# Kernel optimization log

Hardware: AMD Instinct MI355X
Metric: run time of the kernel (lower is better)

Reference implementation:

```python
import jax, jax.numpy as jnp
import numpy as np

B, L, T_ENC = 32, 64, 196
INPUT, EMBED, HIDDEN, VOCAB = 2048, 512, 512, 32000
SCALE = 1.0 / float(512 ** 0.5)


def setup_inputs() -> dict:
    key = jax.random.key(0)
    ks = jax.random.split(key, 24)
    s = 0.05
    embed_table = jax.random.normal(ks[3], (VOCAB, EMBED)) * s
    embed_table = embed_table.at[0].set(0.0)  # padding_idx=0
    d = {
        "features": jax.random.normal(ks[0], (B, INPUT)),
        "captions": jax.random.randint(ks[1], (B, L), 0, VOCAB, dtype=jnp.int32),
        "lengths": jnp.full((B,), L, dtype=jnp.int32),
        "encoder_outputs": jax.random.normal(ks[2], (B, T_ENC, 512)),
        "embed_table": embed_table,
        "ft1_w": jax.random.normal(ks[4], (HIDDEN, INPUT)) * s,
        "ft1_b": jax.random.normal(ks[5], (HIDDEN,)) * s,
        "ft2_w": jax.random.normal(ks[6], (HIDDEN, HIDDEN)) * s,
        "ft2_b": jax.random.normal(ks[7], (HIDDEN,)) * s,
        # torch LSTM gate order: i, f, g, o; layer0 input = embed+512
        "w_ih0": jax.random.normal(ks[8], (4 * HIDDEN, EMBED + 512)) * s,
        "w_hh0": jax.random.normal(ks[9], (4 * HIDDEN, HIDDEN)) * s,
        "b_ih0": jax.random.normal(ks[10], (4 * HIDDEN,)) * s,
        "b_hh0": jax.random.normal(ks[11], (4 * HIDDEN,)) * s,
        "w_ih1": jax.random.normal(ks[12], (4 * HIDDEN, HIDDEN)) * s,
        "w_hh1": jax.random.normal(ks[13], (4 * HIDDEN, HIDDEN)) * s,
        "b_ih1": jax.random.normal(ks[14], (4 * HIDDEN,)) * s,
        "b_hh1": jax.random.normal(ks[15], (4 * HIDDEN,)) * s,
        "fc_w": jax.random.normal(ks[16], (VOCAB, HIDDEN)) * s,
        "fc_b": jax.random.normal(ks[17], (VOCAB,)) * s,
    }
    return d


def _lstm_cell(x, h, c, w_ih, w_hh, b_ih, b_hh):
    g = x @ w_ih.T + h @ w_hh.T + b_ih + b_hh
    i, f, gg, o = jnp.split(g, 4, axis=-1)
    c2 = jax.nn.sigmoid(f) * c + jax.nn.sigmoid(i) * jnp.tanh(gg)
    h2 = jax.nn.sigmoid(o) * jnp.tanh(c2)
    return h2, c2


def reference(features, captions, lengths, encoder_outputs, embed_table,
              ft1_w, ft1_b, ft2_w, ft2_b,
              w_ih0, w_hh0, b_ih0, b_hh0,
              w_ih1, w_hh1, b_ih1, b_hh1,
              fc_w, fc_b):
    # feature extractor (eval mode -> dropout identity)
    f = jax.nn.relu(features @ ft1_w.T + ft1_b)
    f = f @ ft2_w.T + ft2_b                      # [B, H]
    h0 = jnp.stack([f, f])                       # [num_layers, B, H]
    c0 = h0

    emb = embed_table[captions]                  # [B, L, E]
    xs = jnp.swapaxes(emb, 0, 1)                 # [L, B, E]

    def step(carry, w):
        h, c = carry
        q = h[-1]                                             # [B, 512]
        scores = jnp.einsum('bh,bth->bt', q, encoder_outputs) * SCALE
        a = jax.nn.softmax(scores, axis=-1)
        ctx = jnp.einsum('bt,bth->bh', a, encoder_outputs)    # [B, 512]
        x = jnp.concatenate([w, ctx], axis=-1)                # [B, E+512]
        h0n, c0n = _lstm_cell(x, h[0], c[0], w_ih0, w_hh0, b_ih0, b_hh0)
        h1n, c1n = _lstm_cell(h0n, h[1], c[1], w_ih1, w_hh1, b_ih1, b_hh1)
        return (jnp.stack([h0n, h1n]), jnp.stack([c0n, c1n])), h1n

    _, hs = jax.lax.scan(step, (h0, c0), xs)      # hs: [L, B, H]
    logits = jnp.einsum('lbh,vh->lbv', hs, fc_w) + fc_b  # [L, B, V]
    # all lengths == L, so pack_padded_sequence data == time-major flatten
    return logits.reshape(L * B, VOCAB)
```

## Files before the change

### kernel.cpp

```cpp
#include <hip/hip_runtime.h>
#include <hip/hip_bf16.h>

typedef __hip_bfloat16 bf16;
typedef short s8v __attribute__((ext_vector_type(8)));
typedef float f4v __attribute__((ext_vector_type(4)));
typedef unsigned long long u64;
typedef unsigned int u32;

#define B_   32
#define L_   64
#define TENC 196
#define INP  2048
#define H_   512
#define V_   32000
#define NBLK 128

static __device__ __forceinline__ float sigf(float x) { return 1.0f / (1.0f + expf(-x)); }
static __device__ __forceinline__ short f2bs(float x) {
    bf16 h = (bf16)x;
    return *(short*)&h;
}
static __device__ __forceinline__ float b2f(short s) {
    return __uint_as_float(((unsigned int)(unsigned short)s) << 16);
}
static __device__ __forceinline__ u32 packhl(float v) {
    bf16 hi = (bf16)v;
    float r = v - (float)hi;
    bf16 lo = (bf16)r;
    return ((u32)(*(unsigned short*)&hi) << 16) | (u32)(*(unsigned short*)&lo);
}
static __device__ __forceinline__ float ldf(const void* p, size_t i, int f32) {
    if (f32) return ((const float*)p)[i];
    return (float)((const bf16*)p)[i];
}
static __device__ __forceinline__ s8v ld8(const void* p, size_t i, int f32) {
    if (f32) {
        const float* fp = (const float*)p + i;
        float4 a = *(const float4*)fp;
        float4 b = *(const float4*)(fp + 4);
        s8v r;
        r[0] = f2bs(a.x); r[1] = f2bs(a.y); r[2] = f2bs(a.z); r[3] = f2bs(a.w);
        r[4] = f2bs(b.x); r[5] = f2bs(b.y); r[6] = f2bs(b.z); r[7] = f2bs(b.w);
        return r;
    }
    return *(const s8v*)((const bf16*)p + i);
}
static __device__ __forceinline__ s8v ld8lo(const void* p, size_t i, int f32) {
    s8v r = {};
    if (f32) {
        const float* fp = (const float*)p + i;
        float4 a = *(const float4*)fp;
        float4 b = *(const float4*)(fp + 4);
        float v[8] = {a.x, a.y, a.z, a.w, b.x, b.y, b.z, b.w};
        for (int j = 0; j < 8; ++j) {
            bf16 hi = (bf16)v[j];
            bf16 lo = (bf16)(v[j] - (float)hi);
            r[j] = *(short*)&lo;
        }
    }
    return r;
}

static __device__ __forceinline__ u64 ld64coh(const void* p) {
    return __hip_atomic_load((const u64*)p, __ATOMIC_RELAXED, __HIP_MEMORY_SCOPE_AGENT);
}
static __device__ __forceinline__ void st32coh(u32* p, u32 v) {
    __hip_atomic_store(p, v, __ATOMIC_RELAXED, __HIP_MEMORY_SCOPE_AGENT);
}
static __device__ __forceinline__ void st64coh(u32* p, u64 v) {
    __hip_atomic_store((u64*)p, v, __ATOMIC_RELAXED, __HIP_MEMORY_SCOPE_AGENT);
}

static __device__ __forceinline__ void gridbar(int* cnt, int target) {
    asm volatile("s_waitcnt vmcnt(0)" ::: "memory");
    __syncthreads();
    if (threadIdx.x == 0) {
        __hip_atomic_fetch_add(cnt, 1, __ATOMIC_RELAXED, __HIP_MEMORY_SCOPE_AGENT);
        while (__hip_atomic_load(cnt, __ATOMIC_RELAXED, __HIP_MEMORY_SCOPE_AGENT) < target)
            __builtin_amdgcn_s_sleep(1);
    }
    __syncthreads();
}

static __device__ __forceinline__ void issue32(const u32* St, int tid, u64* f) {
    int b0 = (tid >> 7), k = (tid & 127) * 4;
    #pragma unroll
    for (int q = 0; q < 16; ++q) {
        const u32* s = St + (2 * q + b0) * H_ + k;
        f[2 * q]     = ld64coh(s);
        f[2 * q + 1] = ld64coh(s + 2);
    }
}
static __device__ __forceinline__ void stage_write(const u64* f, int tid, short (*A)[520]) {
    int b0 = (tid >> 7), k = (tid & 127) * 4;
    #pragma unroll
    for (int q = 0; q < 16; ++q) {
        u32 v0 = (u32)f[2 * q],     v1 = (u32)(f[2 * q] >> 32);
        u32 v2 = (u32)f[2 * q + 1], v3 = (u32)(f[2 * q + 1] >> 32);
        int b = 2 * q + b0;
        uint2 hi, lo;
        hi.x = (v0 >> 16) | (v1 & 0xffff0000u);
        hi.y = (v2 >> 16) | (v3 & 0xffff0000u);
        lo.x = (v0 & 0xffffu) | (v1 << 16);
        lo.y = (v2 & 0xffffu) | (v3 << 16);
        *(uint2*)&A[2 * b][k]     = hi;
        *(uint2*)&A[2 * b + 1][k] = lo;
    }
}
static __device__ __forceinline__ f4v mfma_half(const short (*W)[1048], const short (*A)[520],
                                                int mrow, int nlo, int kq, int koff, f4v acc) {
    #pragma unroll
    for (int kk = 0; kk < 16; ++kk) {
        s8v a = *(const s8v*)&A[mrow][kk * 32 + kq];
        s8v b = *(const s8v*)&W[nlo][koff + kk * 32 + kq];
        acc = __builtin_amdgcn_mfma_f32_16x16x32_bf16(a, b, acc, 0, 0, 0);
    }
    return acc;
}

__global__ __launch_bounds__(256) void k_detect(const void* __restrict__ feat,
                                                int* __restrict__ flag) {
    __shared__ float red[256];
    const unsigned short* p = (const unsigned short*)feat;
    float mx = 0.f;
    for (int i = threadIdx.x; i < 65536; i += 256) {
        unsigned int u = ((unsigned int)p[i]) << 16;
        float v = __uint_as_float(u);
        mx = fmaxf(mx, fabsf(v));
    }
    red[threadIdx.x] = mx;
    __syncthreads();
    for (int s = 128; s; s >>= 1) {
        if (threadIdx.x < s) red[threadIdx.x] = fmaxf(red[threadIdx.x], red[threadIdx.x + s]);
        __syncthreads();
    }
    if (threadIdx.x == 0) flag[0] = (red[0] > 1e4f) ? 1 : 0;
}

__global__ __launch_bounds__(256) void k_prep(const int* __restrict__ dflag,
                                              const void* __restrict__ enc,
                                              const void* __restrict__ w_ih0, const void* __restrict__ w_hh0,
                                              const void* __restrict__ w_ih1, const void* __restrict__ w_hh1,
                                              const void* __restrict__ b_ih0, const void* __restrict__ b_hh0,
                                              const void* __restrict__ b_ih1, const void* __restrict__ b_hh1,
                                              bf16* __restrict__ enc16,
                                              bf16* __restrict__ Wp0, bf16* __restrict__ Wp1,
                                              float* __restrict__ bias0, float* __restrict__ bias1,
                                              int* __restrict__ bar) {
    int f32 = *dflag;
    int gid = blockIdx.x * 256 + threadIdx.x;
    if (gid == 0) bar[0] = 0;
    const int GE = (B_ * TENC * H_) / 8;
    const int GW = (2048 * 1024) / 8;
    int stride = gridDim.x * 256;
    for (int g = gid; g < GE + 2 * GW; g += stride) {
        if (g < GE) {
            *(s8v*)(enc16 + (size_t)g * 8) = ld8(enc, (size_t)g * 8, f32);
        } else if (g < GE + GW) {
            int gg = g - GE; int j = gg >> 7; int k = (gg & 127) * 8;
            s8v v = (k < 512) ? ld8(w_ih0, (size_t)j * 1024 + 512 + k, f32)
                              : ld8(w_hh0, (size_t)j * 512 + (k - 512), f32);
            *(s8v*)(Wp0 + (size_t)j * 1024 + k) = v;
        } else {
            int gg = g - GE - GW; int j = gg >> 7; int k = (gg & 127) * 8;
            s8v v = (k < 512) ? ld8(w_ih1, (size_t)j * 512 + k, f32)
                              : ld8(w_hh1, (size_t)j * 512 + (k - 512), f32);
            *(s8v*)(Wp1 + (size_t)j * 1024 + k) = v;
        }
    }
    for (int j = gid; j < 2048; j += stride) {
        bias0[j] = ldf(b_ih0, j, f32) + ldf(b_hh0, j, f32);
        bias1[j] = ldf(b_ih1, j, f32) + ldf(b_hh1, j, f32);
    }
}

__global__ __launch_bounds__(256) void k_gemb(const int* __restrict__ dflag,
                                              const int* __restrict__ captions,
                                              const void* __restrict__ embed,
                                              const void* __restrict__ w_ih0,
                                              float* __restrict__ Gemb) {
    __shared__ short As[128][40];
    __shared__ short Bs[128][40];
    int f32 = *dflag;
    int n0 = blockIdx.x * 128;
    int m0 = blockIdx.y * 128;
    int tid = threadIdx.x, lane = tid & 63, wv = tid >> 6;
    int wm = wv >> 1, wn = wv & 1;
    f4v acc[16] = {};
    for (int k0 = 0; k0 < 512; k0 += 32) {
        for (int s = tid; s < 512; s += 256) {
            int r = s >> 2, cs = (s & 3) * 8;
            int R = m0 + r, e = R >> 1, part = R & 1;
            int b = e & 31, tt = e >> 5;
            size_t ei = (size_t)captions[b * L_ + tt] * H_ + k0 + cs;
            *(s8v*)&As[r][cs] = part ? ld8lo(embed, ei, f32) : ld8(embed, ei, f32);
        }
        for (int s = tid; s < 512; s += 256) {
            int r = s >> 2, cs = (s & 3) * 8;
            *(s8v*)&Bs[r][cs] = ld8(w_ih0, (size_t)(n0 + r) * 1024 + k0 + cs, f32);
        }
        __syncthreads();
        int kq = (lane >> 4) * 8;
        s8v af[4], bfv[4];
        for (int i = 0; i < 4; ++i) af[i]  = *(const s8v*)&As[wm * 64 + i * 16 + (lane & 15)][kq];
        for (int i = 0; i < 4; ++i) bfv[i] = *(const s8v*)&Bs[wn * 64 + i * 16 + (lane & 15)][kq];
        for (int mi = 0; mi < 4; ++mi)
            for (int ni = 0; ni < 4; ++ni)
                acc[mi * 4 + ni] = __builtin_amdgcn_mfma_f32_16x16x32_bf16(af[mi], bfv[ni], acc[mi * 4 + ni], 0, 0, 0);
        __syncthreads();
    }
    int n = lane & 15, quad = lane >> 4;
    for (int ni = 0; ni < 4; ++ni) {
        int col = n0 + wn * 64 + ni * 16 + n;
        for (int mi = 0; mi < 4; ++mi) {
            f4v a = acc[mi * 4 + ni];
            int rowbase = m0 + wm * 64 + mi * 16 + quad * 4;
            int e0 = rowbase >> 1;
            Gemb[(size_t)e0 * 2048 + col]       = a[0] + a[1];
            Gemb[(size_t)(e0 + 1) * 2048 + col] = a[2] + a[3];
        }
    }
}

__global__ __launch_bounds__(256) void k_feat1(const int* __restrict__ dflag,
                                               const void* __restrict__ feat,
                                               const void* __restrict__ w,
                                               const void* __restrict__ bias,
                                               float* __restrict__ t1) {
    int f32 = *dflag;
    int wid = (blockIdx.x * 256 + threadIdx.x) >> 6;
    int lane = threadIdx.x & 63;
    int b = wid >> 9, o = wid & 511;
    float acc = 0.f;
    for (int k = lane; k < INP; k += 64)
        acc += ldf(feat, (size_t)b * INP + k, f32) * ldf(w, (size_t)o * INP + k, f32);
    for (int off = 32; off; off >>= 1) acc += __shfl_down(acc, off, 64);
    if (lane == 0) {
        acc += ldf(bias, o, f32);
        t1[b * H_ + o] = acc > 0.f ? acc : 0.f;
    }
}

__global__ __launch_bounds__(256) void k_feat2(const int* __restrict__ dflag,
                                               const float* __restrict__ t1,
                                               const void* __restrict__ w,
                                               const void* __restrict__ bias,
                                               float* __restrict__ c0, float* __restrict__ c1,
                                               u32* __restrict__ h0A, u32* __restrict__ h1A) {
    int f32 = *dflag;
    int wid = (blockIdx.x * 256 + threadIdx.x) >> 6;
    int lane = threadIdx.x & 63;
    int b = wid >> 9, o = wid & 511;
    float acc = 0.f;
    for (int k = lane; k < H_; k += 64)
        acc += t1[b * H_ + k] * ldf(w, (size_t)o * H_ + k, f32);
    for (int off = 32; off; off >>= 1) acc += __shfl_down(acc, off, 64);
    if (lane == 0) {
        float v = acc + ldf(bias, o, f32);
        int idx = b * H_ + o;
        c0[idx] = v; c1[idx] = v;
        u32 pk = packhl(v);
        h0A[idx] = pk; h1A[idx] = pk;
    }
}

__global__ __launch_bounds__(256, 1) void k_recur(
        const bf16* __restrict__ enc16,
        const bf16* __restrict__ Wp0, const bf16* __restrict__ Wp1,
        const float* __restrict__ bias0, const float* __restrict__ bias1,
        const float* __restrict__ Gemb,
        const float* __restrict__ c0i, const float* __restrict__ c1i,
        u32* __restrict__ h0A, u32* __restrict__ h0B,
        u32* __restrict__ h1A, u32* __restrict__ h1B,
        u32* __restrict__ ctxp,
        bf16* __restrict__ hs, int* __restrict__ bar) {
    __shared__ short Asm[64][520];
    __shared__ short Wsm[2][16][1048];
    __shared__ float qs[H_];
    __shared__ float sc[256];
    __shared__ float wred[8];
    __shared__ float ep[4][4][32];
    const float SCALE = 0.04419417382415922f;
    int blk = blockIdx.x, tid = threadIdx.x;
    int lane = tid & 63, wv = tid >> 6;
    int u0 = blk * 4;
    int mrow = wv * 16 + (lane & 15);
    int kq = (lane >> 4) * 8;
    int nlo = lane & 15;
    int quad = lane >> 4;
    int b0i = wv * 8 + quad * 2;
    int eb = tid & 31, eu = (tid >> 5) & 3, ej = u0 + eu;
    int epi = tid < 128;

    for (int cell = 0; cell < 2; ++cell) {
        const bf16* Wp = cell ? Wp1 : Wp0;
        for (int s = tid; s < 2048; s += 256) {
            int r = s >> 7, cc = (s & 127) * 8;
            size_t j = (size_t)((r >> 2) * H_ + u0 + (r & 3));
            *(s8v*)&Wsm[cell][r][cc] = *(const s8v*)(Wp + j * 1024 + cc);
        }
    }
    float c0r = 0.f, c1r = 0.f;
    float bi0 = 0, bf0 = 0, bg0 = 0, bo0 = 0, bi1 = 0, bf1 = 0, bg1 = 0, bo1 = 0;
    if (epi) {
        c0r = c0i[eb * H_ + ej]; c1r = c1i[eb * H_ + ej];
        bi0 = bias0[ej]; bf0 = bias0[512 + ej]; bg0 = bias0[1024 + ej]; bo0 = bias0[1536 + ej];
        bi1 = bias1[ej]; bf1 = bias1[512 + ej]; bg1 = bias1[1024 + ej]; bo1 = bias1[1536 + ej];
    }
    __syncthreads();
    int nbar = 0;

    for (int t = 0; t < L_; ++t) {
        int p = t & 1;
        const u32* h0p = p ? h0B : h0A;  u32* h0n = p ? h0A : h0B;
        const u32* h1p = p ? h1B : h1A;  u32* h1n = p ? h1A : h1B;

        u64 fA[32];
        issue32(h0p, tid, fA);
        f4v accB = {};
        if (blk < B_) {
            int b = blk;
            {
                u64 v = ld64coh(h1p + b * H_ + 2 * tid);
                u32 v0 = (u32)v, v1 = (u32)(v >> 32);
                qs[2 * tid]     = b2f((short)(v0 >> 16)) + b2f((short)(v0 & 0xffffu));
                qs[2 * tid + 1] = b2f((short)(v1 >> 16)) + b2f((short)(v1 & 0xffffu));
            }
            __syncthreads();
            if (tid < TENC) {
                const bf16* erow = enc16 + ((size_t)b * TENC + tid) * H_;
                float a0 = 0, a1 = 0, a2 = 0, a3 = 0, a4 = 0, a5 = 0, a6 = 0, a7 = 0;
                #pragma unroll 4
                for (int k = 0; k < H_; k += 8) {
                    s8v e8 = *(const s8v*)(erow + k);
                    float4 q0 = *(const float4*)&qs[k];
                    float4 q1 = *(const float4*)&qs[k + 4];
                    a0 += q0.x * b2f(e8[0]); a1 += q0.y * b2f(e8[1]);
                    a2 += q0.z * b2f(e8[2]); a3 += q0.w * b2f(e8[3]);
                    a4 += q1.x * b2f(e8[4]); a5 += q1.y * b2f(e8[5]);
                    a6 += q1.z * b2f(e8[6]); a7 += q1.w * b2f(e8[7]);
                }
                sc[tid] = (((a0 + a1) + (a2 + a3)) + ((a4 + a5) + (a6 + a7))) * SCALE;
            }
            __syncthreads();
            float v = (tid < TENC) ? sc[tid] : -1e30f;
            float m = v;
            #pragma unroll
            for (int off = 32; off; off >>= 1) m = fmaxf(m, __shfl_xor(m, off, 64));
            if (lane == 0) wred[wv] = m;
            __syncthreads();
            m = fmaxf(fmaxf(wred[0], wred[1]), fmaxf(wred[2], wred[3]));
            float e = (tid < TENC) ? expf(v - m) : 0.f;
            float s = e;
            #pragma unroll
            for (int off = 32; off; off >>= 1) s += __shfl_xor(s, off, 64);
            if (lane == 0) wred[4 + wv] = s;
            __syncthreads();
            float inv = 1.0f / ((wred[4] + wred[5]) + (wred[6] + wred[7]));
            if (tid < TENC) sc[tid] = e * inv;
            __syncthreads();
            const bf16* ebase = enc16 + (size_t)b * TENC * H_ + 2 * tid;
            float x0 = 0, x1 = 0, y0 = 0, y1 = 0;
            #pragma unroll 4
            for (int tt = 0; tt < TENC; tt += 2) {
                u32 ua = *(const u32*)(ebase + (size_t)tt * H_);
                u32 ub = *(const u32*)(ebase + (size_t)(tt + 1) * H_);
                float p0 = sc[tt], p1 = sc[tt + 1];
                x0 += p0 * b2f((short)ua); x1 += p0 * b2f((short)(ua >> 16));
                y0 += p1 * b2f((short)ub); y1 += p1 * b2f((short)(ub >> 16));
            }
            u64 pk = ((u64)packhl(x1 + y1) << 32) | (u64)packhl(x0 + y0);
            st64coh(ctxp + b * H_ + 2 * tid, pk);
        }
        stage_write(fA, tid, Asm);
        __syncthreads();
        accB = mfma_half(Wsm[0], Asm, mrow, nlo, kq, 512, accB);
        ++nbar; gridbar(bar, nbar * NBLK);

        {
            u64 fB[32];
            issue32(ctxp, tid, fB);
            float g0 = 0, g1 = 0, g2 = 0, g3 = 0;
            if (epi) {
                size_t ge = (size_t)(t * 32 + eb) * 2048 + ej;
                g0 = Gemb[ge]; g1 = Gemb[ge + 512]; g2 = Gemb[ge + 1024]; g3 = Gemb[ge + 1536];
            }
            u64 fC[32];
            issue32(h1p, tid, fC);
            stage_write(fB, tid, Asm);
            __syncthreads();
            accB = mfma_half(Wsm[0], Asm, mrow, nlo, kq, 0, accB);
            ep[nlo >> 2][nlo & 3][b0i]     = accB[0] + accB[1];
            ep[nlo >> 2][nlo & 3][b0i + 1] = accB[2] + accB[3];
            __syncthreads();
            if (epi) {
                float gi = ep[0][eu][eb] + bi0 + g0;
                float gf = ep[1][eu][eb] + bf0 + g1;
                float gg = ep[2][eu][eb] + bg0 + g2;
                float go = ep[3][eu][eb] + bo0 + g3;
                float c2 = sigf(gf) * c0r + sigf(gi) * tanhf(gg);
                float h2 = sigf(go) * tanhf(c2);
                c0r = c2;
                st32coh(h0n + eb * H_ + ej, packhl(h2));
            }
            stage_write(fC, tid, Asm);
            __syncthreads();
            f4v accC = {};
            accC = mfma_half(Wsm[1], Asm, mrow, nlo, kq, 512, accC);
            ++nbar; gridbar(bar, nbar * NBLK);

            u64 fD[32];
            issue32(h0n, tid, fD);
            stage_write(fD, tid, Asm);
            __syncthreads();
            accC = mfma_half(Wsm[1], Asm, mrow, nlo, kq, 0, accC);
            ep[nlo >> 2][nlo & 3][b0i]     = accC[0] + accC[1];
            ep[nlo >> 2][nlo & 3][b0i + 1] = accC[2] + accC[3];
            __syncthreads();
            if (epi) {
                float gi = ep[0][eu][eb] + bi1;
                float gf = ep[1][eu][eb] + bf1;
                float gg = ep[2][eu][eb] + bg1;
                float go = ep[3][eu][eb] + bo1;
                float c2 = sigf(gf) * c1r + sigf(gi) * tanhf(gg);
                float h2 = sigf(go) * tanhf(c2);
                c1r = c2;
                st32coh(h1n + eb * H_ + ej, packhl(h2));
                hs[(size_t)(t * 32 + eb) * H_ + ej] = (bf16)h2;
            }
            ++nbar; gridbar(bar, nbar * NBLK);
        }
    }
}

__global__ __launch_bounds__(256) void k_vocab(const int* __restrict__ dflag,
                                               const bf16* __restrict__ hs,
                                               const void* __restrict__ fcw,
                                               const void* __restrict__ fcb,
                                               void* __restrict__ out) {
    __shared__ short As[128][40];
    __shared__ short Bs[128][40];
    int f32 = *dflag;
    int m0 = blockIdx.x * 128;
    int n0 = blockIdx.y * 128;
    int tid = threadIdx.x, lane = tid & 63, wv = tid >> 6;
    int wm = wv >> 1, wn = wv & 1;
    f4v acc[16] = {};
    for (int k0 = 0; k0 < 512; k0 += 32) {
        for (int s = tid; s < 512; s += 256) {
            int r = s >> 2, cs = (s & 3) * 8;
            *(s8v*)&As[r][cs] = *(const s8v*)(hs + (size_t)(m0 + r) * 512 + k0 + cs);
        }
        for (int s = tid; s < 512; s += 256) {
            int r = s >> 2, cs = (s & 3) * 8;
            *(s8v*)&Bs[r][cs] = ld8(fcw, (size_t)(n0 + r) * 512 + k0 + cs, f32);
        }
        __syncthreads();
        int kq = (lane >> 4) * 8;
        s8v af[4], bfv[4];
        for (int i = 0; i < 4; ++i) af[i]  = *(const s8v*)&As[wm * 64 + i * 16 + (lane & 15)][kq];
        for (int i = 0; i < 4; ++i) bfv[i] = *(const s8v*)&Bs[wn * 64 + i * 16 + (lane & 15)][kq];
        for (int mi = 0; mi < 4; ++mi)
            for (int ni = 0; ni < 4; ++ni)
                acc[mi * 4 + ni] = __builtin_amdgcn_mfma_f32_16x16x32_bf16(af[mi], bfv[ni], acc[mi * 4 + ni], 0, 0, 0);
        __syncthreads();
    }
    int n = lane & 15, quad = lane >> 4;
    for (int ni = 0; ni < 4; ++ni) {
        int col = n0 + wn * 64 + ni * 16 + n;
        float bias = ldf(fcb, col, f32);
        for (int mi = 0; mi < 4; ++mi) {
            f4v a = acc[mi * 4 + ni];
            for (int rg = 0; rg < 4; ++rg) {
                int row = m0 + wm * 64 + mi * 16 + quad * 4 + rg;
                float v = a[rg] + bias;
                if (f32) ((float*)out)[(size_t)row * V_ + col] = v;
                else     ((bf16*)out)[(size_t)row * V_ + col] = (bf16)v;
            }
        }
    }
}

extern "C" void kernel_launch(void* const* d_in, const int* in_sizes, int n_in,
                              void* d_out, int out_size, void* d_ws, size_t ws_size,
                              hipStream_t stream) {
    const void* features = d_in[0];
    const int*  captions = (const int*)d_in[1];
    const void* enc      = d_in[3];
    const void* embed    = d_in[4];
    const void* ft1w     = d_in[5];
    const void* ft1b     = d_in[6];
    const void* ft2w     = d_in[7];
    const void* ft2b     = d_in[8];
    const void* w_ih0    = d_in[9];
    const void* w_hh0    = d_in[10];
    const void* b_ih0    = d_in[11];
    const void* b_hh0    = d_in[12];
    const void* w_ih1    = d_in[13];
    const void* w_hh1    = d_in[14];
    const void* b_ih1    = d_in[15];
    const void* b_hh1    = d_in[16];
    const void* fcw      = d_in[17];
    const void* fcb      = d_in[18];

    char* ws = (char*)d_ws;
    size_t off = 0;
    float* t1    = (float*)(ws + off); off += 32 * 512 * 4;
    float* c0    = (float*)(ws + off); off += 32 * 512 * 4;
    float* c1    = (float*)(ws + off); off += 32 * 512 * 4;
    u32* h0A     = (u32*)(ws + off); off += 32 * 512 * 4;
    u32* h0B     = (u32*)(ws + off); off += 32 * 512 * 4;
    u32* h1A     = (u32*)(ws + off); off += 32 * 512 * 4;
    u32* h1B     = (u32*)(ws + off); off += 32 * 512 * 4;
    u32* ctxp    = (u32*)(ws + off); off += 32 * 512 * 4;
    bf16* hs     = (bf16*)(ws + off); off += (size_t)2048 * 512 * 2;
    bf16* enc16  = (bf16*)(ws + off); off += (size_t)32 * 196 * 512 * 2;
    bf16* Wp0    = (bf16*)(ws + off); off += (size_t)2048 * 1024 * 2;
    bf16* Wp1    = (bf16*)(ws + off); off += (size_t)2048 * 1024 * 2;
    float* bias0 = (float*)(ws + off); off += 2048 * 4;
    float* bias1 = (float*)(ws + off); off += 2048 * 4;
    float* Gemb  = (float*)(ws + off); off += (size_t)2048 * 2048 * 4;
    int* dflag   = (int*)(ws + off); off += 16;
    int* bar     = (int*)(ws + off); off += 16;

    k_detect<<<1, 256, 0, stream>>>(features, dflag);
    k_prep<<<1024, 256, 0, stream>>>(dflag, enc, w_ih0, w_hh0, w_ih1, w_hh1,
                                     b_ih0, b_hh0, b_ih1, b_hh1,
                                     enc16, Wp0, Wp1, bias0, bias1, bar);
    k_gemb<<<dim3(16, 32), 256, 0, stream>>>(dflag, captions, embed, w_ih0, Gemb);
    k_feat1<<<4096, 256, 0, stream>>>(dflag, features, ft1w, ft1b, t1);
    k_feat2<<<4096, 256, 0, stream>>>(dflag, t1, ft2w, ft2b, c0, c1, h0A, h1A);
    k_recur<<<NBLK, 256, 0, stream>>>(enc16, Wp0, Wp1, bias0, bias1, Gemb,
                                      c0, c1, h0A, h0B, h1A, h1B, ctxp, hs, bar);
    k_vocab<<<dim3(16, 250), 256, 0, stream>>>(dflag, hs, fcw, fcb, (void*)d_out);
}
```

Before: 2.808 ms.

## Replace atomic-counter grid barrier with per-block flag slots and partial waits

The single atomic-add counter barrier is replaced by per-block padded flag slots. Each block stores its step number, and all threads poll the slots in parallel and combine the result with __syncthreads_and. The first barrier of each step now waits only on the 32 blocks that produce the needed data rather than all 128. The aim is to remove contention on one atomic address and shorten waits on the sequential recurrence, at the cost of more polling traffic and more dependence on correct monotonic slot values.

```diff
diff --git a/kernel.cpp b/kernel.cpp
--- a/kernel.cpp
+++ b/kernel.cpp
@@ -14,6 +14,7 @@
 #define H_   512
 #define V_   32000
 #define NBLK 128
+#define SLOTSTRIDE 16
 
 static __device__ __forceinline__ float sigf(float x) { return 1.0f / (1.0f + expf(-x)); }
 static __device__ __forceinline__ short f2bs(float x) {
@@ -71,15 +72,21 @@
     __hip_atomic_store((u64*)p, v, __ATOMIC_RELAXED, __HIP_MEMORY_SCOPE_AGENT);
 }
 
-static __device__ __forceinline__ void gridbar(int* cnt, int target) {
+static __device__ __forceinline__ void slot_arrive(u32* slots, int blk, u32 val) {
     asm volatile("s_waitcnt vmcnt(0)" ::: "memory");
     __syncthreads();
-    if (threadIdx.x == 0) {
-        __hip_atomic_fetch_add(cnt, 1, __ATOMIC_RELAXED, __HIP_MEMORY_SCOPE_AGENT);
-        while (__hip_atomic_load(cnt, __ATOMIC_RELAXED, __HIP_MEMORY_SCOPE_AGENT) < target)
-            __builtin_amdgcn_s_sleep(1);
-    }
-    __syncthreads();
+    if (threadIdx.x == 0)
+        __hip_atomic_store(slots + blk * SLOTSTRIDE, val, __ATOMIC_RELAXED, __HIP_MEMORY_SCOPE_AGENT);
+}
+static __device__ __forceinline__ void slot_wait(const u32* slots, int nslots, u32 val) {
+    int tid = threadIdx.x;
+    for (;;) {
+        u32 v = val;
+        if (tid < nslots)
+            v = __hip_atomic_load(slots + tid * SLOTSTRIDE, __ATOMIC_RELAXED, __HIP_MEMORY_SCOPE_AGENT);
+        if (__syncthreads_and((int)(v >= val))) break;
+        __builtin_amdgcn_s_sleep(1);
+    }
 }
 
 static __device__ __forceinline__ void issue32(const u32* St, int tid, u64* f) {
@@ -146,10 +153,10 @@
                                               bf16* __restrict__ enc16,
                                               bf16* __restrict__ Wp0, bf16* __restrict__ Wp1,
                                               float* __restrict__ bias0, float* __restrict__ bias1,
-                                              int* __restrict__ bar) {
+                                              u32* __restrict__ slots) {
     int f32 = *dflag;
     int gid = blockIdx.x * 256 + threadIdx.x;
-    if (gid == 0) bar[0] = 0;
+    if (gid < NBLK * SLOTSTRIDE) slots[gid] = 0;
     const int GE = (B_ * TENC * H_) / 8;
     const int GW = (2048 * 1024) / 8;
     int stride = gridDim.x * 256;
@@ -273,7 +280,7 @@
         u32* __restrict__ h0A, u32* __restrict__ h0B,
         u32* __restrict__ h1A, u32* __restrict__ h1B,
         u32* __restrict__ ctxp,
-        bf16* __restrict__ hs, int* __restrict__ bar) {
+        bf16* __restrict__ hs, u32* __restrict__ slots) {
     __shared__ short Asm[64][520];
     __shared__ short Wsm[2][16][1048];
     __shared__ float qs[H_];
@@ -308,7 +315,7 @@
         bi1 = bias1[ej]; bf1 = bias1[512 + ej]; bg1 = bias1[1024 + ej]; bo1 = bias1[1536 + ej];
     }
     __syncthreads();
-    int nbar = 0;
+    u32 nbar = 0;
 
     for (int t = 0; t < L_; ++t) {
         int p = t & 1;
@@ -375,7 +382,9 @@
         stage_write(fA, tid, Asm);
         __syncthreads();
         accB = mfma_half(Wsm[0], Asm, mrow, nlo, kq, 512, accB);
-        ++nbar; gridbar(bar, nbar * NBLK);
+        ++nbar;
+        if (blk < B_) slot_arrive(slots, blk, nbar);
+        slot_wait(slots, B_, nbar);
 
         {
             u64 fB[32];
@@ -407,7 +416,9 @@
             __syncthreads();
             f4v accC = {};
             accC = mfma_half(Wsm[1], Asm, mrow, nlo, kq, 512, accC);
-            ++nbar; gridbar(bar, nbar * NBLK);
+            ++nbar;
+            slot_arrive(slots, blk, nbar);
+            slot_wait(slots, NBLK, nbar);
 
             u64 fD[32];
             issue32(h0n, tid, fD);
@@ -428,7 +439,9 @@
                 st32coh(h1n + eb * H_ + ej, packhl(h2));
                 hs[(size_t)(t * 32 + eb) * H_ + ej] = (bf16)h2;
             }
-            ++nbar; gridbar(bar, nbar * NBLK);
+            ++nbar;
+            slot_arrive(slots, blk, nbar);
+            slot_wait(slots, NBLK, nbar);
         }
     }
 }
@@ -521,16 +534,16 @@
     float* bias1 = (float*)(ws + off); off += 2048 * 4;
     float* Gemb  = (float*)(ws + off); off += (size_t)2048 * 2048 * 4;
     int* dflag   = (int*)(ws + off); off += 16;
-    int* bar     = (int*)(ws + off); off += 16;
+    u32* slots   = (u32*)(ws + off); off += NBLK * SLOTSTRIDE * 4;
 
     k_detect<<<1, 256, 0, stream>>>(features, dflag);
     k_prep<<<1024, 256, 0, stream>>>(dflag, enc, w_ih0, w_hh0, w_ih1, w_hh1,
                                      b_ih0, b_hh0, b_ih1, b_hh1,
-                                     enc16, Wp0, Wp1, bias0, bias1, bar);
+                                     enc16, Wp0, Wp1, bias0, bias1, slots);
     k_gemb<<<dim3(16, 32), 256, 0, stream>>>(dflag, captions, embed, w_ih0, Gemb);
     k_feat1<<<4096, 256, 0, stream>>>(dflag, features, ft1w, ft1b, t1);
     k_feat2<<<4096, 256, 0, stream>>>(dflag, t1, ft2w, ft2b, c0, c1, h0A, h1A);
     k_recur<<<NBLK, 256, 0, stream>>>(enc16, Wp0, Wp1, bias0, bias1, Gemb,
-                                      c0, c1, h0A, h0B, h1A, h1B, ctxp, hs, bar);
+                                      c0, c1, h0A, h0B, h1A, h1B, ctxp, hs, slots);
     k_vocab<<<dim3(16, 250), 256, 0, stream>>>(dflag, hs, fcw, fcb, (void*)d_out);
 }
```

New measurement: 2.636 ms. -6.1%, faster.
